# Optimization experiments

Hardware: AMD Instinct MI355X
Metric: run time of the kernel (lower is better)

Reference implementation:

```python
import jax, jax.numpy as jnp
from jax import lax
import numpy as np

KERNEL = 3
PAD = KERNEL // 2


def _normalized_weights(affinity):
    # affinity: [B, 8, H, W] -> 9-tap weights [B, 9, H, W] with center at index 4
    aff_sum = jnp.sum(jnp.abs(affinity), axis=1, keepdims=True)
    aff_norm = affinity / aff_sum
    center = 1.0 - jnp.sum(aff_norm, axis=1, keepdims=True)
    # Original loop uses affinity channels 0..3 for taps before center, 4..7 after
    return jnp.concatenate([aff_norm[:, :4], center, aff_norm[:, 4:]], axis=1)


def setup_inputs() -> dict:
    key = jax.random.key(0)
    k1, k2 = jax.random.split(key)
    B, H, W = 8, 480, 640
    affinity = jax.random.normal(k1, (B, KERNEL * KERNEL - 1, H, W), dtype=jnp.float32)
    feature = jax.random.normal(k2, (B, 1, H, W), dtype=jnp.float32)
    return {"affinity": affinity, "feature": feature, "times": 24}


def reference(affinity, feature, times):
    weights = _normalized_weights(affinity)  # [B, 9, H, W]
    B, C, H, W = feature.shape

    def step(f, _):
        fp = jnp.pad(f, ((0, 0), (0, 0), (PAD, PAD), (PAD, PAD)))
        # 9 shifted views stacked on a tap axis: [B, 9, C, H, W]
        shifts = jnp.stack(
            [fp[:, :, i:i + H, j:j + W] for i in range(KERNEL) for j in range(KERNEL)],
            axis=1,
        )
        f_new = jnp.sum(shifts * weights[:, :, None, :, :], axis=1)
        return f_new, None

    out, _ = lax.scan(step, feature, None, length=times)
    return out
```

## Files before the change

### kernel.cpp

```cpp
#include <hip/hip_runtime.h>
#include <hip/hip_fp16.h>
#include <cstddef>


#define HIMG 480
#define WIMG 640
#define HW   (HIMG * WIMG)
#define BN   8

#define TILE   40
#define TSTEPS 12
#define IH     13
#define WHL    12
#define SW     66
#define PITCH  68
#define NT     512

#define WS_FRAME_B  ((size_t)BN * HW * 4)
#define WS_WA_B     ((size_t)BN * HW * 16)
#define WS_WC_B     ((size_t)BN * HW * 4)
#define WS_NEED     (WS_FRAME_B + WS_WA_B + WS_WC_B)

template <int MODE>
__global__ __launch_bounds__(NT, 4) void affprop12(
    const float* __restrict__ aff,
    __half2* __restrict__ wA,
    float* __restrict__ wC,
    const float* __restrict__ src,
    float* __restrict__ dst)
{
    __shared__ float fA[SW * PITCH];
    __shared__ float fB[SW * PITCH];

    const int tid = threadIdx.x;
    const int ox  = blockIdx.x * TILE;
    const int oy  = blockIdx.y * TILE;
    const int b   = blockIdx.z;

    const float* __restrict__ sb = src + (size_t)b * HW;
    float*       __restrict__ db = dst + (size_t)b * HW;

    for (int i = tid; i < SW * SW; i += NT) {
        int r  = i / SW;
        int c  = i - r * SW;
        int gy = oy - IH + r;
        int gx = ox - IH + c;
        float v = 0.f;
        if ((unsigned)gy < (unsigned)HIMG && (unsigned)gx < (unsigned)WIMG)
            v = sb[gy * WIMG + gx];
        fA[r * PITCH + c] = v;
    }
    for (int i = tid; i < SW * PITCH / 4; i += NT)
        *(float4*)&fB[4 * i] = make_float4(0.f, 0.f, 0.f, 0.f);

    const int c  = tid & 63;
    const int g  = tid >> 6;
    const int sc = c + 1;

    __half2 wv[8][4];
    float   wcc[8];

    #pragma unroll
    for (int i = 0; i < 8; ++i) {
        const int gy = oy - WHL + 8 * g + i;
        const int gx = ox - WHL + c;
        const bool in = (unsigned)gy < (unsigned)HIMG && (unsigned)gx < (unsigned)WIMG;
        const size_t idx = (size_t)b * HW + (size_t)gy * WIMG + gx;

        if (MODE == 1) {
            if (in) {
                union { float4 f4; __half2 h[4]; } u;
                u.f4 = *(const float4*)(wA + 4 * idx);
                wv[i][0] = u.h[0]; wv[i][1] = u.h[1];
                wv[i][2] = u.h[2]; wv[i][3] = u.h[3];
                wcc[i] = wC[idx];
            } else {
                __half2 z = __floats2half2_rn(0.f, 0.f);
                wv[i][0] = z; wv[i][1] = z; wv[i][2] = z; wv[i][3] = z;
                wcc[i] = 0.f;
            }
        } else {
            float w[8];
            float s = 0.f;
            if (in) {
                const float* ap = aff + (size_t)b * 8 * HW + (size_t)gy * WIMG + gx;
                #pragma unroll
                for (int k = 0; k < 8; ++k) { w[k] = ap[(size_t)k * HW]; s += fabsf(w[k]); }
            } else {
                #pragma unroll
                for (int k = 0; k < 8; ++k) w[k] = 0.f;
                s = 1.f;
            }
            float rr  = in ? 1.0f / s : 0.f;
            float acc = 0.f;
            #pragma unroll
            for (int k = 0; k < 8; ++k) { w[k] *= rr; acc += w[k]; }

            union { float4 f4; __half2 h[4]; } u;
            u.h[0] = __floats2half2_rn(w[0], w[1]);
            u.h[1] = __floats2half2_rn(w[2], w[3]);
            u.h[2] = __floats2half2_rn(w[4], w[5]);
            u.h[3] = __floats2half2_rn(w[6], w[7]);
            wv[i][0] = u.h[0]; wv[i][1] = u.h[1];
            wv[i][2] = u.h[2]; wv[i][3] = u.h[3];
            wcc[i] = in ? 1.0f - acc : 0.f;

            if (MODE == 0) {
                if ((unsigned)(gy - oy) < (unsigned)TILE &&
                    (unsigned)(gx - ox) < (unsigned)TILE) {
                    *(float4*)(wA + 4 * idx) = u.f4;
                    wC[idx] = wcc[i];
                }
            }
        }
    }
    __syncthreads();

    const float* fin = fA;
    float*       fo  = fB;

    #pragma unroll 1
    for (int s = 0; s < TSTEPS; ++s) {
        const float* rp = fin + (8 * g) * PITCH + c;
        float a0 = rp[0], a1 = rp[1], a2 = rp[2];
        rp += PITCH;
        float b0 = rp[0], b1 = rp[1], b2 = rp[2];
        float* wp = fo + (8 * g + 1) * PITCH + sc;

        #pragma unroll
        for (int i = 0; i < 8; ++i) {
            rp += PITCH;
            float c0 = rp[0], c1 = rp[1], c2 = rp[2];

            float o = wcc[i] * b1
                + __low2float (wv[i][0]) * a0
                + __high2float(wv[i][0]) * a1
                + __low2float (wv[i][1]) * a2
                + __high2float(wv[i][1]) * b0
                + __low2float (wv[i][2]) * b2
                + __high2float(wv[i][2]) * c0
                + __low2float (wv[i][3]) * c1
                + __high2float(wv[i][3]) * c2;

            *wp = o;
            wp += PITCH;
            a0 = b0; a1 = b1; a2 = b2;
            b0 = c0; b1 = c1; b2 = c2;
        }
        __syncthreads();
        const float* t = fin; fin = fo; fo = (float*)t;
    }

    for (int i = tid; i < TILE * (TILE / 4); i += NT) {
        int r  = i / (TILE / 4);
        int c4 = (i - r * (TILE / 4)) * 4;
        const float* p = fin + (IH + r) * PITCH + IH + c4;
        float4 v = make_float4(p[0], p[1], p[2], p[3]);
        *(float4*)&db[(size_t)(oy + r) * WIMG + ox + c4] = v;
    }
}

extern "C" void kernel_launch(void* const* d_in, const int* in_sizes, int n_in,
                              void* d_out, int out_size, void* d_ws, size_t ws_size,
                              hipStream_t stream)
{
    const float* aff  = (const float*)d_in[0];
    const float* feat = (const float*)d_in[1];
    float* out = (float*)d_out;

    char* ws = (char*)d_ws;
    float*   wsFrame = (float*)ws;
    __half2* wA      = (__half2*)(ws + WS_FRAME_B);
    float*   wC      = (float*)(ws + WS_FRAME_B + WS_WA_B);

    dim3 blk(NT, 1, 1);
    dim3 grd(WIMG / TILE, HIMG / TILE, BN);

    if (ws_size >= WS_NEED) {
        affprop12<0><<<grd, blk, 0, stream>>>(aff, wA, wC, feat, wsFrame);
        affprop12<1><<<grd, blk, 0, stream>>>(aff, wA, wC, wsFrame, out);
    } else {
        affprop12<2><<<grd, blk, 0, stream>>>(aff, nullptr, nullptr, feat, wsFrame);
        affprop12<2><<<grd, blk, 0, stream>>>(aff, nullptr, nullptr, wsFrame, out);
    }
}
```

Before: 220.9 us.

## Use taller 40x80 tiles with 13 rows per wave and skip dead halo rows

```diff
diff --git a/kernel.cpp b/kernel.cpp
--- a/kernel.cpp
+++ b/kernel.cpp
@@ -8,11 +8,14 @@
 #define HW   (HIMG * WIMG)
 #define BN   8
 
-#define TILE   40
+#define TILEW  40
+#define TILEH  80
+#define NROW   13
 #define TSTEPS 12
 #define IH     13
 #define WHL    12
-#define SW     66
+#define SROWS  106
+#define SCOLS  66
 #define PITCH  68
 #define NT     512
 
@@ -22,27 +25,27 @@
 #define WS_NEED     (WS_FRAME_B + WS_WA_B + WS_WC_B)
 
 template <int MODE>
-__global__ __launch_bounds__(NT, 4) void affprop12(
+__global__ __launch_bounds__(NT, 2) void affprop12(
     const float* __restrict__ aff,
     __half2* __restrict__ wA,
     float* __restrict__ wC,
     const float* __restrict__ src,
     float* __restrict__ dst)
 {
-    __shared__ float fA[SW * PITCH];
-    __shared__ float fB[SW * PITCH];
+    __shared__ float fA[SROWS * PITCH];
+    __shared__ float fB[SROWS * PITCH];
 
     const int tid = threadIdx.x;
-    const int ox  = blockIdx.x * TILE;
-    const int oy  = blockIdx.y * TILE;
+    const int ox  = blockIdx.x * TILEW;
+    const int oy  = blockIdx.y * TILEH;
     const int b   = blockIdx.z;
 
     const float* __restrict__ sb = src + (size_t)b * HW;
     float*       __restrict__ db = dst + (size_t)b * HW;
 
-    for (int i = tid; i < SW * SW; i += NT) {
-        int r  = i / SW;
-        int c  = i - r * SW;
+    for (int i = tid; i < SROWS * SCOLS; i += NT) {
+        int r  = i / SCOLS;
+        int c  = i - r * SCOLS;
         int gy = oy - IH + r;
         int gx = ox - IH + c;
         float v = 0.f;
@@ -50,19 +53,19 @@
             v = sb[gy * WIMG + gx];
         fA[r * PITCH + c] = v;
     }
-    for (int i = tid; i < SW * PITCH / 4; i += NT)
+    for (int i = tid; i < SROWS * PITCH / 4; i += NT)
         *(float4*)&fB[4 * i] = make_float4(0.f, 0.f, 0.f, 0.f);
 
     const int c  = tid & 63;
-    const int g  = tid >> 6;
+    const int w  = tid >> 6;
     const int sc = c + 1;
 
-    __half2 wv[8][4];
-    float   wcc[8];
+    __half2 wv[NROW][4];
+    float   wcc[NROW];
 
     #pragma unroll
-    for (int i = 0; i < 8; ++i) {
-        const int gy = oy - WHL + 8 * g + i;
+    for (int i = 0; i < NROW; ++i) {
+        const int gy = oy - WHL + NROW * w + i;
         const int gx = ox - WHL + c;
         const bool in = (unsigned)gy < (unsigned)HIMG && (unsigned)gx < (unsigned)WIMG;
         const size_t idx = (size_t)b * HW + (size_t)gy * WIMG + gx;
@@ -80,34 +83,34 @@
                 wcc[i] = 0.f;
             }
         } else {
-            float w[8];
+            float wt[8];
             float s = 0.f;
             if (in) {
                 const float* ap = aff + (size_t)b * 8 * HW + (size_t)gy * WIMG + gx;
                 #pragma unroll
-                for (int k = 0; k < 8; ++k) { w[k] = ap[(size_t)k * HW]; s += fabsf(w[k]); }
+                for (int k = 0; k < 8; ++k) { wt[k] = ap[(size_t)k * HW]; s += fabsf(wt[k]); }
             } else {
                 #pragma unroll
-                for (int k = 0; k < 8; ++k) w[k] = 0.f;
+                for (int k = 0; k < 8; ++k) wt[k] = 0.f;
                 s = 1.f;
             }
             float rr  = in ? 1.0f / s : 0.f;
             float acc = 0.f;
             #pragma unroll
-            for (int k = 0; k < 8; ++k) { w[k] *= rr; acc += w[k]; }
+            for (int k = 0; k < 8; ++k) { wt[k] *= rr; acc += wt[k]; }
 
             union { float4 f4; __half2 h[4]; } u;
-            u.h[0] = __floats2half2_rn(w[0], w[1]);
-            u.h[1] = __floats2half2_rn(w[2], w[3]);
-            u.h[2] = __floats2half2_rn(w[4], w[5]);
-            u.h[3] = __floats2half2_rn(w[6], w[7]);
+            u.h[0] = __floats2half2_rn(wt[0], wt[1]);
+            u.h[1] = __floats2half2_rn(wt[2], wt[3]);
+            u.h[2] = __floats2half2_rn(wt[4], wt[5]);
+            u.h[3] = __floats2half2_rn(wt[6], wt[7]);
             wv[i][0] = u.h[0]; wv[i][1] = u.h[1];
             wv[i][2] = u.h[2]; wv[i][3] = u.h[3];
             wcc[i] = in ? 1.0f - acc : 0.f;
 
             if (MODE == 0) {
-                if ((unsigned)(gy - oy) < (unsigned)TILE &&
-                    (unsigned)(gx - ox) < (unsigned)TILE) {
+                if ((unsigned)(gy - oy) < (unsigned)TILEH &&
+                    (unsigned)(gx - ox) < (unsigned)TILEW) {
                     *(float4*)(wA + 4 * idx) = u.f4;
                     wC[idx] = wcc[i];
                 }
@@ -121,39 +124,42 @@
 
     #pragma unroll 1
     for (int s = 0; s < TSTEPS; ++s) {
-        const float* rp = fin + (8 * g) * PITCH + c;
-        float a0 = rp[0], a1 = rp[1], a2 = rp[2];
-        rp += PITCH;
-        float b0 = rp[0], b1 = rp[1], b2 = rp[2];
-        float* wp = fo + (8 * g + 1) * PITCH + sc;
+        const bool live = (NROW * w + NROW >= s + 1) && (NROW * w + 1 <= 104 - s);
+        if (live) {
+            const float* rp = fin + (NROW * w) * PITCH + c;
+            float a0 = rp[0], a1 = rp[1], a2 = rp[2];
+            rp += PITCH;
+            float b0 = rp[0], b1 = rp[1], b2 = rp[2];
+            float* wp = fo + (NROW * w + 1) * PITCH + sc;
 
-        #pragma unroll
-        for (int i = 0; i < 8; ++i) {
-            rp += PITCH;
-            float c0 = rp[0], c1 = rp[1], c2 = rp[2];
+            #pragma unroll
+            for (int i = 0; i < NROW; ++i) {
+                rp += PITCH;
+                float c0 = rp[0], c1 = rp[1], c2 = rp[2];
 
-            float o = wcc[i] * b1
-                + __low2float (wv[i][0]) * a0
-                + __high2float(wv[i][0]) * a1
-                + __low2float (wv[i][1]) * a2
-                + __high2float(wv[i][1]) * b0
-                + __low2float (wv[i][2]) * b2
-                + __high2float(wv[i][2]) * c0
-                + __low2float (wv[i][3]) * c1
-                + __high2float(wv[i][3]) * c2;
+                float o = wcc[i] * b1
+                    + __low2float (wv[i][0]) * a0
+                    + __high2float(wv[i][0]) * a1
+                    + __low2float (wv[i][1]) * a2
+                    + __high2float(wv[i][1]) * b0
+                    + __low2float (wv[i][2]) * b2
+                    + __high2float(wv[i][2]) * c0
+                    + __low2float (wv[i][3]) * c1
+                    + __high2float(wv[i][3]) * c2;
 
-            *wp = o;
-            wp += PITCH;
-            a0 = b0; a1 = b1; a2 = b2;
-            b0 = c0; b1 = c1; b2 = c2;
+                *wp = o;
+                wp += PITCH;
+                a0 = b0; a1 = b1; a2 = b2;
+                b0 = c0; b1 = c1; b2 = c2;
+            }
         }
         __syncthreads();
         const float* t = fin; fin = fo; fo = (float*)t;
     }
 
-    for (int i = tid; i < TILE * (TILE / 4); i += NT) {
-        int r  = i / (TILE / 4);
-        int c4 = (i - r * (TILE / 4)) * 4;
+    for (int i = tid; i < TILEH * (TILEW / 4); i += NT) {
+        int r  = i / (TILEW / 4);
+        int c4 = (i - r * (TILEW / 4)) * 4;
         const float* p = fin + (IH + r) * PITCH + IH + c4;
         float4 v = make_float4(p[0], p[1], p[2], p[3]);
         *(float4*)&db[(size_t)(oy + r) * WIMG + ox + c4] = v;
@@ -174,7 +180,7 @@
     float*   wC      = (float*)(ws + WS_FRAME_B + WS_WA_B);
 
     dim3 blk(NT, 1, 1);
-    dim3 grd(WIMG / TILE, HIMG / TILE, BN);
+    dim3 grd(WIMG / TILEW, HIMG / TILEH, BN);
 
     if (ws_size >= WS_NEED) {
         affprop12<0><<<grd, blk, 0, stream>>>(aff, wA, wC, feat, wsFrame);
```

New measurement: 253.8 us. 1.15x slower.
